# Optimization experiments

Measured on AMD Instinct MI355X. Metric: run time of the kernel, lower is better.

The kernel has to match this reference:

```python
import jax, jax.numpy as jnp
import numpy as np

HEADS = 8
K = 3            # kernel_size per axis
RPB = 2 * K - 1  # rel-pos-bias extent per axis
EPS = 1e-5


def _nbr(dim, k):
    # NATTEN-style clamped window: shift window to stay fully inside [0, dim)
    q = jnp.arange(dim)
    start = jnp.clip(q - k // 2, 0, dim - k)
    nbr = start[:, None] + jnp.arange(k)[None, :]       # (dim, k) neighbor coords
    rel = nbr - q[:, None] + (k - 1)                    # (dim, k) in [0, 2k-2]
    return nbr, rel


def _instance_norm(x):
    # InstanceNorm3d, affine=False: normalize over spatial dims per (B, C)
    m = jnp.mean(x, axis=(2, 3, 4), keepdims=True)
    v = jnp.var(x, axis=(2, 3, 4), keepdims=True)
    return (x - m) * jax.lax.rsqrt(v + EPS)


def setup_inputs() -> dict:
    key = jax.random.key(0)
    ks = jax.random.split(key, 10)
    B, C, H, W, Z = 1, 128, 32, 32, 32
    Cf = 4 * C
    s = 0.02
    return {
        "x": jax.random.normal(ks[0], (B, C, H, W, Z), jnp.float32),
        "w_qkv": jax.random.normal(ks[1], (3 * C, C), jnp.float32) * s,
        "b_qkv": jnp.zeros((3 * C,), jnp.float32),
        "rpb": jax.random.normal(ks[2], (HEADS, RPB, RPB, RPB), jnp.float32) * s,
        "w_proj": jax.random.normal(ks[3], (C, C), jnp.float32) * s,
        "b_proj": jnp.zeros((C,), jnp.float32),
        "w_ffn1": jax.random.normal(ks[4], (Cf, C), jnp.float32) * s,
        "b_ffn1": jnp.zeros((Cf,), jnp.float32),
        "w_ffn2": jax.random.normal(ks[5], (C, Cf), jnp.float32) * s,
        "b_ffn2": jnp.zeros((C,), jnp.float32),
    }


def reference(x, w_qkv, b_qkv, rpb, w_proj, b_proj, w_ffn1, b_ffn1, w_ffn2, b_ffn2):
    B, C, H, W, Z = x.shape
    hd = C // HEADS
    N = H * W * Z
    KK = K ** 3

    # ---- SAM: 3D neighborhood self-attention ----
    xt = x.reshape(B, C, N).transpose(0, 2, 1)                 # (B, N, C)
    qkv = xt @ w_qkv.T + b_qkv                                  # (B, N, 3C)
    q, k_, v = jnp.split(qkv, 3, axis=-1)
    split = lambda t: t.reshape(B, N, HEADS, hd).transpose(0, 2, 1, 3)  # (B, h, N, d)
    q, k_, v = split(q), split(k_), split(v)

    nh, rh = _nbr(H, K)
    nw, rw = _nbr(W, K)
    nz, rz = _nbr(Z, K)
    # flat neighbor token index per (h, w, z, kh, kw, kz)
    nbr = ((nh[:, None, None, :, None, None] * W
            + nw[None, :, None, None, :, None]) * Z
           + nz[None, None, :, None, None, :]).reshape(N, KK)   # (N, 27)
    # flat rel-pos-bias index
    bidx = ((rh[:, None, None, :, None, None] * RPB
             + rw[None, :, None, None, :, None]) * RPB
            + rz[None, None, :, None, None, :]).reshape(N, KK)  # (N, 27)

    kg = k_[:, :, nbr]                                          # (B, h, N, 27, d)
    vg = v[:, :, nbr]                                           # (B, h, N, 27, d)
    bias = rpb.reshape(HEADS, RPB ** 3)[:, bidx]                # (h, N, 27)

    scale = jnp.asarray(hd, x.dtype) ** -0.5
    attn = jnp.einsum('bhnd,bhnkd->bhnk', q * scale, kg) + bias
    attn = jax.nn.softmax(attn, axis=-1)
    out = jnp.einsum('bhnk,bhnkd->bhnd', attn, vg)              # (B, h, N, d)
    out = out.transpose(0, 2, 1, 3).reshape(B, N, C) @ w_proj.T + b_proj
    x5 = out.transpose(0, 2, 1).reshape(B, C, H, W, Z)

    # ---- norm_in ----
    x5 = _instance_norm(x5)

    # ---- FFN (mmcv-style, GELU, residual identity) ----
    t = x5.reshape(B, C, N).transpose(0, 2, 1)                  # (B, N, C)
    t = t + (jax.nn.gelu(t @ w_ffn1.T + b_ffn1) @ w_ffn2.T + b_ffn2)
    x5 = t.transpose(0, 2, 1).reshape(B, C, H, W, Z)

    # ---- norm_out ----
    return _instance_norm(x5)
```

## Files before the change

kernel.cpp:

```cpp
#include <hip/hip_runtime.h>
#include <hip/hip_bf16.h>
#include <math.h>

#define NPOS 32768
#define CCH  128
#define C3   384
#define CF   512

typedef __attribute__((ext_vector_type(8))) short short8;
typedef __attribute__((ext_vector_type(4))) float f32x4;

__device__ inline float bf2f(unsigned short u) {
    union { unsigned int i; float f; } x; x.i = ((unsigned int)u) << 16; return x.f;
}
__device__ inline unsigned short f2bf(float f) {
    union { float f; unsigned int i; } x; x.f = f;
    unsigned int r = x.i + 0x7FFFu + ((x.i >> 16) & 1u);
    return (unsigned short)(r >> 16);
}
__device__ inline float lo_bf(unsigned int u) {
    union { unsigned int i; float f; } x; x.i = u << 16; return x.f;
}
__device__ inline float hi_bf(unsigned int u) {
    union { unsigned int i; float f; } x; x.i = u & 0xffff0000u; return x.f;
}

template<bool GELU, bool RES, bool WF32, bool WBF>
__global__ __launch_bounds__(256) void gemm_mfma(
    const unsigned short* __restrict__ A, const unsigned short* __restrict__ B,
    const float* __restrict__ bias, const unsigned short* __restrict__ res,
    float* __restrict__ outf, unsigned short* __restrict__ outb,
    int M, int Nout, int K)
{
    __shared__ alignas(16) unsigned short As[128 * 40];
    __shared__ alignas(16) unsigned short Bs[128 * 40];

    const int tid  = threadIdx.x;
    const int lane = tid & 63;
    const int wave = tid >> 6;
    const int wm = wave & 1, wn = wave >> 1;
    const int row0 = blockIdx.y * 128;
    const int col0 = blockIdx.x * 128;

    const f32x4 fzero = {0.f, 0.f, 0.f, 0.f};
    f32x4 acc[4][4];
    #pragma unroll
    for (int i = 0; i < 4; ++i)
        #pragma unroll
        for (int j = 0; j < 4; ++j) acc[i][j] = fzero;

    const int lr = lane & 15;
    const int lk = (lane >> 4) * 8;

    for (int kt = 0; kt < K; kt += 32) {
        #pragma unroll
        for (int it = 0; it < 2; ++it) {
            const int c = tid + it * 256;
            const int r = c >> 2;
            const int p = (c & 3) * 8;
            *(uint4*)&As[r * 40 + p] = *(const uint4*)&A[(size_t)(row0 + r) * K + kt + p];
            *(uint4*)&Bs[r * 40 + p] = *(const uint4*)&B[(size_t)(col0 + r) * K + kt + p];
        }
        __syncthreads();
        short8 af[4], bfr[4];
        #pragma unroll
        for (int i = 0; i < 4; ++i)
            af[i]  = *(const short8*)&As[(wm * 64 + i * 16 + lr) * 40 + lk];
        #pragma unroll
        for (int j = 0; j < 4; ++j)
            bfr[j] = *(const short8*)&Bs[(wn * 64 + j * 16 + lr) * 40 + lk];
        #pragma unroll
        for (int i = 0; i < 4; ++i)
            #pragma unroll
            for (int j = 0; j < 4; ++j)
                acc[i][j] = __builtin_amdgcn_mfma_f32_16x16x32_bf16(
                                af[i], bfr[j], acc[i][j], 0, 0, 0);
        __syncthreads();
    }

    const int gr0 = row0 + wm * 64 + (lane >> 4) * 4;
    const int gc0 = col0 + wn * 64 + lr;
    #pragma unroll
    for (int j = 0; j < 4; ++j) {
        const int gc = gc0 + j * 16;
        const float bv = bias[gc];
        #pragma unroll
        for (int i = 0; i < 4; ++i) {
            #pragma unroll
            for (int r = 0; r < 4; ++r) {
                const int gr = gr0 + i * 16 + r;
                float v = acc[i][j][r] + bv;
                if (GELU) {
                    const float g = 0.7978845608028654f * (v + 0.044715f * v * v * v);
                    const float e = __expf(2.f * g);
                    v = v * (e / (e + 1.f));
                }
                if (RES)  v += bf2f(res[(size_t)gr * Nout + gc]);
                if (WF32) outf[(size_t)gr * Nout + gc] = v;
                if (WBF)  outb[(size_t)gr * Nout + gc] = f2bf(v);
            }
        }
    }
}

__global__ __launch_bounds__(256) void attn_tiled(
    const unsigned short* __restrict__ qkv, const float* __restrict__ rpb,
    unsigned short* __restrict__ out)
{
    __shared__ unsigned int ksu[288 * 8];
    __shared__ unsigned int vsu[288 * 8];
    __shared__ unsigned int qsu[32 * 8];
    __shared__ float logits[32 * 29];
    __shared__ float rpbs[125];

    const int t  = threadIdx.x;
    const int line = ((blockIdx.x & 7) << 7) + (blockIdx.x >> 3);
    const int h  = blockIdx.y;
    const int w0 = line & 31, h0 = line >> 5;
    const int n0 = (h0 << 10) + (w0 << 5);
    const int sh0 = min(max(h0 - 1, 0), 29);
    const int sw0 = min(max(w0 - 1, 0), 29);
    const int rh_off = sh0 - h0 + 2;
    const int rw_off = sw0 - w0 + 2;

    if (t < 64) {
        const int pos = t >> 1, part = t & 1;
        const uint4 raw = *(const uint4*)&qkv[(size_t)(n0 + pos) * C3 + h * 16 + part * 8];
        *(uint4*)&qsu[pos * 8 + part * 4] = raw;
    } else if (t < 192) {
        const int i = t - 64;
        if (i < 125) rpbs[i] = rpb[h * 125 + i];
    }
    for (int c = t; c < 1152; c += 256) {
        const int p = c >> 2, part = c & 3;
        const int ihw = p >> 5, z = p & 31;
        const int ih = (ihw * 11) >> 5;
        const int iw = ihw - 3 * ih;
        const int n = ((sh0 + ih) << 10) + ((sw0 + iw) << 5) + z;
        const uint4 raw = *(const uint4*)&qkv[(size_t)n * C3 + CCH + (part >> 1) * CCH
                                              + h * 16 + (part & 1) * 8];
        unsigned int* d = ((part < 2) ? ksu : vsu) + p * 8 + (part & 1) * 4;
        *(uint4*)d = raw;
    }
    __syncthreads();

    {
        const int q = t >> 3, j = t & 7;
        const int sz = min(max(q - 1, 0), 29);
        const int rz_off = sz - q + 2;
        float qf[16];
        #pragma unroll
        for (int d2 = 0; d2 < 8; ++d2) {
            const unsigned int u = qsu[q * 8 + d2];
            qf[2 * d2] = lo_bf(u); qf[2 * d2 + 1] = hi_bf(u);
        }
        for (int kk = j; kk < 27; kk += 8) {
            const int ihw = kk / 3, dz = kk - 3 * ihw;
            const int ih = ihw / 3,  iw = ihw - 3 * ih;
            const int p = ihw * 32 + sz + dz;
            float a = 0.f;
            #pragma unroll
            for (int d2 = 0; d2 < 8; ++d2) {
                const unsigned int u = ksu[p * 8 + d2];
                a += qf[2 * d2] * lo_bf(u) + qf[2 * d2 + 1] * hi_bf(u);
            }
            const int bidx = ((ih + rh_off) * 5 + (iw + rw_off)) * 5 + (dz + rz_off);
            logits[q * 29 + kk] = a * 0.25f + rpbs[bidx];
        }
    }
    __syncthreads();

    if (t < 32) {
        float mx = -1e30f;
        #pragma unroll
        for (int kk = 0; kk < 27; ++kk) mx = fmaxf(mx, logits[t * 29 + kk]);
        float s = 0.f;
        #pragma unroll
        for (int kk = 0; kk < 27; ++kk) {
            const float e = __expf(logits[t * 29 + kk] - mx);
            logits[t * 29 + kk] = e; s += e;
        }
        const float inv = 1.f / s;
        #pragma unroll
        for (int kk = 0; kk < 27; ++kk) logits[t * 29 + kk] *= inv;
    }
    __syncthreads();

    {
        const int q = t >> 3, d2 = t & 7;
        const int sz = min(max(q - 1, 0), 29);
        float ax = 0.f, ay = 0.f;
        #pragma unroll
        for (int kk = 0; kk < 27; ++kk) {
            const int p = (kk / 3) * 32 + sz + (kk % 3);
            const float w = logits[q * 29 + kk];
            const unsigned int u = vsu[p * 8 + d2];
            ax += w * lo_bf(u); ay += w * hi_bf(u);
        }
        const unsigned int o = ((unsigned int)f2bf(ay) << 16) | (unsigned int)f2bf(ax);
        *(unsigned int*)&out[(size_t)(n0 + q) * CCH + h * 16 + d2 * 2] = o;
    }
}

__global__ __launch_bounds__(256, 2) void proj_stats_kernel(
    const unsigned short* __restrict__ attnO,
    const unsigned short* __restrict__ wproj,
    const float* __restrict__ b_proj,
    unsigned short* __restrict__ x5b,
    float* __restrict__ stats)
{
    __shared__ alignas(16) unsigned short As[64 * 136];
    __shared__ alignas(16) unsigned short Bs[128 * 136];
    __shared__ float red[256];

    const int t    = threadIdx.x;
    const int lane = t & 63;
    const int wn   = t >> 6;
    const int lr = lane & 15;
    const int lg = lane >> 4;
    const int lk = lg * 8;
    const int n0 = blockIdx.x * 64;

    red[t] = 0.f;
    #pragma unroll
    for (int it = 0; it < 4; ++it) {
        const int idx = t + it * 256;
        const int row = idx >> 4, rem = (idx & 15) * 8;
        *(uint4*)&As[row * 136 + rem] = *(const uint4*)&attnO[(size_t)(n0 + row) * CCH + rem];
    }
    #pragma unroll
    for (int it = 0; it < 8; ++it) {
        const int idx = t + it * 256;
        const int row = idx >> 4, rem = (idx & 15) * 8;
        *(uint4*)&Bs[row * 136 + rem] = *(const uint4*)&wproj[row * CCH + rem];
    }
    __syncthreads();

    const f32x4 fzero = {0.f, 0.f, 0.f, 0.f};
    f32x4 acc[4][2];
    #pragma unroll
    for (int i = 0; i < 4; ++i)
        #pragma unroll
        for (int j = 0; j < 2; ++j) acc[i][j] = fzero;

    #pragma unroll
    for (int ks = 0; ks < 4; ++ks) {
        short8 af[4], bfr[2];
        #pragma unroll
        for (int i = 0; i < 4; ++i)
            af[i]  = *(const short8*)&As[(i * 16 + lr) * 136 + ks * 32 + lk];
        #pragma unroll
        for (int j = 0; j < 2; ++j)
            bfr[j] = *(const short8*)&Bs[(wn * 32 + j * 16 + lr) * 136 + ks * 32 + lk];
        #pragma unroll
        for (int i = 0; i < 4; ++i)
            #pragma unroll
            for (int j = 0; j < 2; ++j)
                acc[i][j] = __builtin_amdgcn_mfma_f32_16x16x32_bf16(
                                af[i], bfr[j], acc[i][j], 0, 0, 0);
    }

    #pragma unroll
    for (int j = 0; j < 2; ++j) {
        const int gc = wn * 32 + j * 16 + lr;
        const float bv = b_proj[gc];
        float s = 0.f, q = 0.f;
        #pragma unroll
        for (int i = 0; i < 4; ++i)
            #pragma unroll
            for (int r = 0; r < 4; ++r) {
                const int gr = i * 16 + lg * 4 + r;
                const float v = acc[i][j][r] + bv;
                s += v; q += v * v;
                x5b[(size_t)(n0 + gr) * CCH + gc] = f2bf(v);
            }
        atomicAdd(&red[gc], s);
        atomicAdd(&red[128 + gc], q);
    }
    __syncthreads();
    if (t < 128) {
        atomicAdd(&stats[t],       red[t]);
        atomicAdd(&stats[128 + t], red[128 + t]);
    }
}

__global__ __launch_bounds__(256, 2) void ffn_fused_kernel(
    const unsigned short* __restrict__ x5b,
    const unsigned short* __restrict__ w1,
    const float* __restrict__ b1,
    const unsigned short* __restrict__ w2,
    const float* __restrict__ b2,
    float* __restrict__ stats,
    float* __restrict__ tT)
{
    __shared__ alignas(16) unsigned short As[64 * 136];
    __shared__ alignas(16) unsigned short Ws[128 * 136];
    __shared__ alignas(16) unsigned short Hs[64 * 136];
    __shared__ float red[256];
    __shared__ float ms[128];
    __shared__ float rss[128];

    const int t    = threadIdx.x;
    const int lane = t & 63;
    const int wn   = t >> 6;
    const int lr = lane & 15;
    const int lg = lane >> 4;
    const int lk = lg * 8;
    const int n0 = blockIdx.x * 64;
    const float invN = 1.f / (float)NPOS;
    const f32x4 fzero = {0.f, 0.f, 0.f, 0.f};

    red[t] = 0.f;
    if (t < 128) {
        const float m = stats[t] * invN;
        const float v = stats[128 + t] * invN - m * m;
        ms[t]  = m;
        rss[t] = rsqrtf(v + 1e-5f);
    }
    uint4 pw[8];
    #pragma unroll
    for (int it = 0; it < 8; ++it) {
        const int idx = t + it * 256;
        const int row = idx >> 4, rem = (idx & 15) * 8;
        pw[it] = *(const uint4*)&w1[(size_t)row * CCH + rem];
    }
    uint4 px[4];
    #pragma unroll
    for (int it = 0; it < 4; ++it) {
        const int idx = t + it * 256;
        const int row = idx >> 4, c0 = (idx & 15) * 8;
        px[it] = *(const uint4*)&x5b[(size_t)(n0 + row) * CCH + c0];
    }
    __syncthreads();

    #pragma unroll
    for (int it = 0; it < 4; ++it) {
        const int idx = t + it * 256;
        const int row = idx >> 4, c0 = (idx & 15) * 8;
        unsigned int u[4] = {px[it].x, px[it].y, px[it].z, px[it].w};
        #pragma unroll
        for (int p = 0; p < 4; ++p) {
            const int c = c0 + 2 * p;
            const float a = (lo_bf(u[p]) - ms[c])     * rss[c];
            const float b = (hi_bf(u[p]) - ms[c + 1]) * rss[c + 1];
            u[p] = ((unsigned int)f2bf(b) << 16) | (unsigned int)f2bf(a);
        }
        uint4 w; w.x = u[0]; w.y = u[1]; w.z = u[2]; w.w = u[3];
        *(uint4*)&As[row * 136 + c0] = w;
    }

    f32x4 acc[4][2];
    #pragma unroll
    for (int i = 0; i < 4; ++i)
        #pragma unroll
        for (int j = 0; j < 2; ++j) acc[i][j] = fzero;

    #pragma unroll 1
    for (int cc = 0; cc < 4; ++cc) {
        #pragma unroll
        for (int it = 0; it < 8; ++it) {
            const int idx = t + it * 256;
            const int row = idx >> 4, rem = (idx & 15) * 8;
            *(uint4*)&Ws[row * 136 + rem] = pw[it];
        }
        #pragma unroll
        for (int it = 0; it < 8; ++it) {
            const int idx = t + it * 256;
            const int row = idx >> 4, rem = (idx & 15) * 8;
            pw[it] = *(const uint4*)&w2[(size_t)row * CF + cc * 128 + rem];
        }
        __syncthreads();

        f32x4 hacc[4][2];
        #pragma unroll
        for (int i = 0; i < 4; ++i)
            #pragma unroll
            for (int j = 0; j < 2; ++j) hacc[i][j] = fzero;
        #pragma unroll
        for (int ks = 0; ks < 4; ++ks) {
            short8 af[4], bfr[2];
            #pragma unroll
            for (int i = 0; i < 4; ++i)
                af[i]  = *(const short8*)&As[(i * 16 + lr) * 136 + ks * 32 + lk];
            #pragma unroll
            for (int j = 0; j < 2; ++j)
                bfr[j] = *(const short8*)&Ws[(wn * 32 + j * 16 + lr) * 136 + ks * 32 + lk];
            #pragma unroll
            for (int i = 0; i < 4; ++i)
                #pragma unroll
                for (int j = 0; j < 2; ++j)
                    hacc[i][j] = __builtin_amdgcn_mfma_f32_16x16x32_bf16(
                                    af[i], bfr[j], hacc[i][j], 0, 0, 0);
        }
        #pragma unroll
        for (int j = 0; j < 2; ++j) {
            const int gc = wn * 32 + j * 16 + lr;
            const float bv = b1[cc * 128 + gc];
            #pragma unroll
            for (int i = 0; i < 4; ++i)
                #pragma unroll
                for (int r = 0; r < 4; ++r) {
                    float v = hacc[i][j][r] + bv;
                    const float g = 0.7978845608028654f * (v + 0.044715f * v * v * v);
                    const float e = __expf(2.f * g);
                    v = v * (e / (e + 1.f));
                    Hs[(i * 16 + lg * 4 + r) * 136 + gc] = f2bf(v);
                }
        }
        __syncthreads();

        #pragma unroll
        for (int it = 0; it < 8; ++it) {
            const int idx = t + it * 256;
            const int row = idx >> 4, rem = (idx & 15) * 8;
            *(uint4*)&Ws[row * 136 + rem] = pw[it];
        }
        if (cc < 3) {
            #pragma unroll
            for (int it = 0; it < 8; ++it) {
                const int idx = t + it * 256;
                const int row = idx >> 4, rem = (idx & 15) * 8;
                pw[it] = *(const uint4*)&w1[(size_t)((cc + 1) * 128 + row) * CCH + rem];
            }
        }
        __syncthreads();

        #pragma unroll
        for (int ks = 0; ks < 4; ++ks) {
            short8 af[4], bfr[2];
            #pragma unroll
            for (int i = 0; i < 4; ++i)
                af[i]  = *(const short8*)&Hs[(i * 16 + lr) * 136 + ks * 32 + lk];
            #pragma unroll
            for (int j = 0; j < 2; ++j)
                bfr[j] = *(const short8*)&Ws[(wn * 32 + j * 16 + lr) * 136 + ks * 32 + lk];
            #pragma unroll
            for (int i = 0; i < 4; ++i)
                #pragma unroll
                for (int j = 0; j < 2; ++j)
                    acc[i][j] = __builtin_amdgcn_mfma_f32_16x16x32_bf16(
                                    af[i], bfr[j], acc[i][j], 0, 0, 0);
        }
        __syncthreads();
    }

    #pragma unroll
    for (int j = 0; j < 2; ++j) {
        const int gc = wn * 32 + j * 16 + lr;
        const float bv = b2[gc];
        float s = 0.f, q = 0.f;
        #pragma unroll
        for (int i = 0; i < 4; ++i)
            #pragma unroll
            for (int r = 0; r < 4; ++r) {
                const int gr = i * 16 + lg * 4 + r;
                const float v = acc[i][j][r] + bv + bf2f(As[gr * 136 + gc]);
                acc[i][j][r] = v;
                s += v; q += v * v;
            }
        atomicAdd(&red[gc], s);
        atomicAdd(&red[128 + gc], q);
    }
    __syncthreads();
    if (t < 128) {
        atomicAdd(&stats[256 + t], red[t]);
        atomicAdd(&stats[384 + t], red[128 + t]);
    }

    float* tr = (float*)Ws;
    #pragma unroll
    for (int j = 0; j < 2; ++j) {
        const int gc = wn * 32 + j * 16 + lr;
        #pragma unroll
        for (int i = 0; i < 4; ++i)
            #pragma unroll
            for (int r = 0; r < 4; ++r) {
                const int gr = i * 16 + lg * 4 + r;
                tr[gc * 68 + gr] = acc[i][j][r];
            }
    }
    __syncthreads();
    #pragma unroll
    for (int it = 0; it < 8; ++it) {
        const int idx = t + it * 256;
        const int c = idx >> 4, ch = (idx & 15) * 4;
        float4 o4;
        o4.x = tr[c * 68 + ch + 0];
        o4.y = tr[c * 68 + ch + 1];
        o4.z = tr[c * 68 + ch + 2];
        o4.w = tr[c * 68 + ch + 3];
        *(float4*)&tT[(size_t)c * NPOS + n0 + ch] = o4;
    }
}

__global__ __launch_bounds__(256) void norm2_apply_kernel(
    const float* __restrict__ tT, const float* __restrict__ stats,
    float* __restrict__ out)
{
    const int i = blockIdx.x * 256 + threadIdx.x;
    const size_t o = (size_t)i * 4;
    const int c = (int)(o >> 15);
    const float invN = 1.f / (float)NPOS;
    const float m  = stats[256 + c] * invN;
    const float vr = stats[384 + c] * invN - m * m;
    const float rs = rsqrtf(vr + 1e-5f);
    float4 v = ((const float4*)tT)[i];
    v.x = (v.x - m) * rs;
    v.y = (v.y - m) * rs;
    v.z = (v.z - m) * rs;
    v.w = (v.w - m) * rs;
    ((float4*)out)[i] = v;
}

__global__ __launch_bounds__(256) void prep_kernel(
    const float* __restrict__ wq, const float* __restrict__ wp,
    const float* __restrict__ w1, const float* __restrict__ w2,
    unsigned short* __restrict__ wq_b, unsigned short* __restrict__ wp_b,
    unsigned short* __restrict__ w1_b, unsigned short* __restrict__ w2_b,
    float* __restrict__ stats)
{
    const int i = blockIdx.x * 256 + threadIdx.x;
    if (blockIdx.x == 0) {
        stats[threadIdx.x] = 0.f;
        stats[threadIdx.x + 256] = 0.f;
    }
    const float* src; unsigned short* dst; int off;
    if (i < 12288)      { src = wq; dst = wq_b; off = i; }
    else if (i < 16384) { src = wp; dst = wp_b; off = i - 12288; }
    else if (i < 32768) { src = w1; dst = w1_b; off = i - 16384; }
    else                { src = w2; dst = w2_b; off = i - 32768; }
    const float4 v = ((const float4*)src)[off];
    ushort4 o;
    o.x = f2bf(v.x); o.y = f2bf(v.y); o.z = f2bf(v.z); o.w = f2bf(v.w);
    ((ushort4*)dst)[off] = o;
}

__global__ __launch_bounds__(256) void transpose_x_kernel(
    const float* __restrict__ x, unsigned short* __restrict__ xt)
{
    __shared__ float tile[32][33];
    const int n0 = blockIdx.x * 32;
    const int c0 = blockIdx.y * 32;
    const int tx = threadIdx.x & 31;
    const int ty = threadIdx.x >> 5;
    for (int i = ty; i < 32; i += 8)
        tile[i][tx] = x[(size_t)(c0 + i) * NPOS + n0 + tx];
    __syncthreads();
    for (int i = ty; i < 32; i += 8)
        xt[(size_t)(n0 + i) * CCH + c0 + tx] = f2bf(tile[tx][i]);
}

extern "C" void kernel_launch(void* const* d_in, const int* in_sizes, int n_in,
                              void* d_out, int out_size, void* d_ws, size_t ws_size,
                              hipStream_t stream)
{
    const float* x      = (const float*)d_in[0];
    const float* w_qkv  = (const float*)d_in[1];
    const float* b_qkv  = (const float*)d_in[2];
    const float* rpb    = (const float*)d_in[3];
    const float* w_proj = (const float*)d_in[4];
    const float* b_proj = (const float*)d_in[5];
    const float* w_ffn1 = (const float*)d_in[6];
    const float* b_ffn1 = (const float*)d_in[7];
    const float* w_ffn2 = (const float*)d_in[8];
    const float* b_ffn2 = (const float*)d_in[9];
    float* out = (float*)d_out;

    char* ws = (char*)d_ws;
    unsigned short* xt_bf    = (unsigned short*)(ws + 0);
    unsigned short* qkv_bf   = (unsigned short*)(ws + 8388608);
    unsigned short* attnO_bf = (unsigned short*)(ws + 33554432);
    unsigned short* x5_bf    = (unsigned short*)(ws + 41943040);
    float*          tT       = (float*)(ws + 50331648);
    unsigned short* wqkv_bf  = (unsigned short*)(ws + 83886080);
    unsigned short* wproj_bf = (unsigned short*)(ws + 83984384);
    unsigned short* wffn1_bf = (unsigned short*)(ws + 84017152);
    unsigned short* wffn2_bf = (unsigned short*)(ws + 84148224);
    float*          stats    = (float*)(ws + 84279296);

    prep_kernel<<<192, 256, 0, stream>>>(w_qkv, w_proj, w_ffn1, w_ffn2,
                                         wqkv_bf, wproj_bf, wffn1_bf, wffn2_bf, stats);
    transpose_x_kernel<<<dim3(NPOS / 32, CCH / 32), 256, 0, stream>>>(x, xt_bf);

    gemm_mfma<false, false, false, true><<<dim3(C3 / 128, NPOS / 128), 256, 0, stream>>>(
        xt_bf, wqkv_bf, b_qkv, nullptr, nullptr, qkv_bf, NPOS, C3, CCH);

    attn_tiled<<<dim3(1024, 8), 256, 0, stream>>>(qkv_bf, rpb, attnO_bf);

    proj_stats_kernel<<<NPOS / 64, 256, 0, stream>>>(
        attnO_bf, wproj_bf, b_proj, x5_bf, stats);

    ffn_fused_kernel<<<NPOS / 64, 256, 0, stream>>>(
        x5_bf, wffn1_bf, b_ffn1, wffn2_bf, b_ffn2, stats, tT);

    norm2_apply_kernel<<<(NPOS * CCH / 4) / 256, 256, 0, stream>>>(tT, stats, out);
}
```

Before: 213.4 us.

## Load weight MFMA fragments directly from global memory, dropping LDS staging

In the proj and FFN kernels, weight B-fragments now come straight from global memory (L2/L1-cached) into registers, so the shared-memory weight tiles and their copy-in passes go away. The proj kernel also reads its activation fragments directly from global memory. The FFN kernel reuses one LDS pool for the activation, hidden and transpose buffers, and the launch_bounds occupancy hint is dropped. This cuts LDS traffic and barriers and may raise occupancy, at the cost of uncoalesced, redundant global loads: every block rereads the weights with 16-byte strided accesses.

```diff
diff --git a/kernel.cpp b/kernel.cpp
--- a/kernel.cpp
+++ b/kernel.cpp
@@ -202,15 +202,13 @@
     }
 }
 
-__global__ __launch_bounds__(256, 2) void proj_stats_kernel(
+__global__ __launch_bounds__(256) void proj_stats_kernel(
     const unsigned short* __restrict__ attnO,
     const unsigned short* __restrict__ wproj,
     const float* __restrict__ b_proj,
     unsigned short* __restrict__ x5b,
     float* __restrict__ stats)
 {
-    __shared__ alignas(16) unsigned short As[64 * 136];
-    __shared__ alignas(16) unsigned short Bs[128 * 136];
     __shared__ float red[256];
 
     const int t    = threadIdx.x;
@@ -222,19 +220,13 @@
     const int n0 = blockIdx.x * 64;
 
     red[t] = 0.f;
-    #pragma unroll
-    for (int it = 0; it < 4; ++it) {
-        const int idx = t + it * 256;
-        const int row = idx >> 4, rem = (idx & 15) * 8;
-        *(uint4*)&As[row * 136 + rem] = *(const uint4*)&attnO[(size_t)(n0 + row) * CCH + rem];
-    }
-    #pragma unroll
-    for (int it = 0; it < 8; ++it) {
-        const int idx = t + it * 256;
-        const int row = idx >> 4, rem = (idx & 15) * 8;
-        *(uint4*)&Bs[row * 136 + rem] = *(const uint4*)&wproj[row * CCH + rem];
-    }
-    __syncthreads();
+
+    short8 wf[2][4];
+    #pragma unroll
+    for (int j = 0; j < 2; ++j)
+        #pragma unroll
+        for (int ks = 0; ks < 4; ++ks)
+            wf[j][ks] = *(const short8*)&wproj[(wn * 32 + j * 16 + lr) * CCH + ks * 32 + lk];
 
     const f32x4 fzero = {0.f, 0.f, 0.f, 0.f};
     f32x4 acc[4][2];
@@ -245,20 +237,18 @@
 
     #pragma unroll
     for (int ks = 0; ks < 4; ++ks) {
-        short8 af[4], bfr[2];
-        #pragma unroll
-        for (int i = 0; i < 4; ++i)
-            af[i]  = *(const short8*)&As[(i * 16 + lr) * 136 + ks * 32 + lk];
-        #pragma unroll
-        for (int j = 0; j < 2; ++j)
-            bfr[j] = *(const short8*)&Bs[(wn * 32 + j * 16 + lr) * 136 + ks * 32 + lk];
+        short8 af[4];
+        #pragma unroll
+        for (int i = 0; i < 4; ++i)
+            af[i] = *(const short8*)&attnO[(size_t)(n0 + i * 16 + lr) * CCH + ks * 32 + lk];
         #pragma unroll
         for (int i = 0; i < 4; ++i)
             #pragma unroll
             for (int j = 0; j < 2; ++j)
                 acc[i][j] = __builtin_amdgcn_mfma_f32_16x16x32_bf16(
-                                af[i], bfr[j], acc[i][j], 0, 0, 0);
-    }
+                                af[i], wf[j][ks], acc[i][j], 0, 0, 0);
+    }
+    __syncthreads();
 
     #pragma unroll
     for (int j = 0; j < 2; ++j) {
@@ -284,7 +274,7 @@
     }
 }
 
-__global__ __launch_bounds__(256, 2) void ffn_fused_kernel(
+__global__ __launch_bounds__(256) void ffn_fused_kernel(
     const unsigned short* __restrict__ x5b,
     const unsigned short* __restrict__ w1,
     const float* __restrict__ b1,
@@ -293,9 +283,9 @@
     float* __restrict__ stats,
     float* __restrict__ tT)
 {
-    __shared__ alignas(16) unsigned short As[64 * 136];
-    __shared__ alignas(16) unsigned short Ws[128 * 136];
-    __shared__ alignas(16) unsigned short Hs[64 * 136];
+    __shared__ alignas(16) unsigned short pool[2 * 17408];
+    unsigned short* As = pool;
+    unsigned short* Hs = pool + 17408;
     __shared__ float red[256];
     __shared__ float ms[128];
     __shared__ float rss[128];
@@ -317,13 +307,6 @@
         ms[t]  = m;
         rss[t] = rsqrtf(v + 1e-5f);
     }
-    uint4 pw[8];
-    #pragma unroll
-    for (int it = 0; it < 8; ++it) {
-        const int idx = t + it * 256;
-        const int row = idx >> 4, rem = (idx & 15) * 8;
-        pw[it] = *(const uint4*)&w1[(size_t)row * CCH + rem];
-    }
     uint4 px[4];
     #pragma unroll
     for (int it = 0; it < 4; ++it) {
@@ -348,6 +331,7 @@
         uint4 w; w.x = u[0]; w.y = u[1]; w.z = u[2]; w.w = u[3];
         *(uint4*)&As[row * 136 + c0] = w;
     }
+    __syncthreads();
 
     f32x4 acc[4][2];
     #pragma unroll
@@ -357,19 +341,13 @@
 
     #pragma unroll 1
     for (int cc = 0; cc < 4; ++cc) {
-        #pragma unroll
-        for (int it = 0; it < 8; ++it) {
-            const int idx = t + it * 256;
-            const int row = idx >> 4, rem = (idx & 15) * 8;
-            *(uint4*)&Ws[row * 136 + rem] = pw[it];
-        }
-        #pragma unroll
-        for (int it = 0; it < 8; ++it) {
-            const int idx = t + it * 256;
-            const int row = idx >> 4, rem = (idx & 15) * 8;
-            pw[it] = *(const uint4*)&w2[(size_t)row * CF + cc * 128 + rem];
-        }
-        __syncthreads();
+        short8 w1f[2][4];
+        #pragma unroll
+        for (int j = 0; j < 2; ++j)
+            #pragma unroll
+            for (int ks = 0; ks < 4; ++ks)
+                w1f[j][ks] = *(const short8*)&w1[
+                    (size_t)(cc * 128 + wn * 32 + j * 16 + lr) * CCH + ks * 32 + lk];
 
         f32x4 hacc[4][2];
         #pragma unroll
@@ -378,20 +356,26 @@
             for (int j = 0; j < 2; ++j) hacc[i][j] = fzero;
         #pragma unroll
         for (int ks = 0; ks < 4; ++ks) {
-            short8 af[4], bfr[2];
+            short8 af[4];
             #pragma unroll
             for (int i = 0; i < 4; ++i)
-                af[i]  = *(const short8*)&As[(i * 16 + lr) * 136 + ks * 32 + lk];
-            #pragma unroll
-            for (int j = 0; j < 2; ++j)
-                bfr[j] = *(const short8*)&Ws[(wn * 32 + j * 16 + lr) * 136 + ks * 32 + lk];
+                af[i] = *(const short8*)&As[(i * 16 + lr) * 136 + ks * 32 + lk];
             #pragma unroll
             for (int i = 0; i < 4; ++i)
                 #pragma unroll
                 for (int j = 0; j < 2; ++j)
                     hacc[i][j] = __builtin_amdgcn_mfma_f32_16x16x32_bf16(
-                                    af[i], bfr[j], hacc[i][j], 0, 0, 0);
-        }
+                                    af[i], w1f[j][ks], hacc[i][j], 0, 0, 0);
+        }
+
+        short8 w2f[2][4];
+        #pragma unroll
+        for (int j = 0; j < 2; ++j)
+            #pragma unroll
+            for (int ks = 0; ks < 4; ++ks)
+                w2f[j][ks] = *(const short8*)&w2[
+                    (size_t)(wn * 32 + j * 16 + lr) * CF + cc * 128 + ks * 32 + lk];
+
         #pragma unroll
         for (int j = 0; j < 2; ++j) {
             const int gc = wn * 32 + j * 16 + lr;
@@ -410,36 +394,17 @@
         __syncthreads();
 
         #pragma unroll
-        for (int it = 0; it < 8; ++it) {
-            const int idx = t + it * 256;
-            const int row = idx >> 4, rem = (idx & 15) * 8;
-            *(uint4*)&Ws[row * 136 + rem] = pw[it];
-        }
-        if (cc < 3) {
-            #pragma unroll
-            for (int it = 0; it < 8; ++it) {
-                const int idx = t + it * 256;
-                const int row = idx >> 4, rem = (idx & 15) * 8;
-                pw[it] = *(const uint4*)&w1[(size_t)((cc + 1) * 128 + row) * CCH + rem];
-            }
-        }
-        __syncthreads();
-
-        #pragma unroll
         for (int ks = 0; ks < 4; ++ks) {
-            short8 af[4], bfr[2];
+            short8 af[4];
             #pragma unroll
             for (int i = 0; i < 4; ++i)
-                af[i]  = *(const short8*)&Hs[(i * 16 + lr) * 136 + ks * 32 + lk];
-            #pragma unroll
-            for (int j = 0; j < 2; ++j)
-                bfr[j] = *(const short8*)&Ws[(wn * 32 + j * 16 + lr) * 136 + ks * 32 + lk];
+                af[i] = *(const short8*)&Hs[(i * 16 + lr) * 136 + ks * 32 + lk];
             #pragma unroll
             for (int i = 0; i < 4; ++i)
                 #pragma unroll
                 for (int j = 0; j < 2; ++j)
                     acc[i][j] = __builtin_amdgcn_mfma_f32_16x16x32_bf16(
-                                    af[i], bfr[j], acc[i][j], 0, 0, 0);
+                                    af[i], w2f[j][ks], acc[i][j], 0, 0, 0);
         }
         __syncthreads();
     }
@@ -467,7 +432,7 @@
         atomicAdd(&stats[384 + t], red[128 + t]);
     }
 
-    float* tr = (float*)Ws;
+    float* tr = (float*)pool;
     #pragma unroll
     for (int j = 0; j < 2; ++j) {
         const int gc = wn * 32 + j * 16 + lr;
```

New measurement: 200.9 us. 5.8% less time.
